# Performance work log

Measured on AMD Instinct MI355X. Metric: run time of the kernel, lower is better.

## Reference

```python
import jax, jax.numpy as jnp
import numpy as np

B, C, H, W = 64, 64, 64, 64
KD = 64  # kernel_dim == res == dim (required by the torch reshapes)


def _ln(t, g, b, eps=1e-5):
    mu = jnp.mean(t, axis=-1, keepdims=True)
    var = jnp.var(t, axis=-1, keepdims=True)
    return (t - mu) * jax.lax.rsqrt(var + eps) * g + b


def _cos_map(n, kd):
    i = jnp.arange(n, dtype=jnp.float32)[:, None]
    j = jnp.arange(kd, dtype=jnp.float32)[None, :]
    return jnp.cos(i * j * jnp.pi / n) / kd


def setup_inputs() -> dict:
    key = jax.random.key(0)
    ks = jax.random.split(key, 6)
    s = 0.02
    return {
        "x": jax.random.normal(ks[0], (B, C, H, W), jnp.float32),
        "freq_embed": jax.random.normal(ks[1], (H, W, C), jnp.float32),
        "g_k": jnp.ones((C,), jnp.float32), "b_k": jnp.zeros((C,), jnp.float32),
        "Wk": jax.random.normal(ks[2], (C, KD), jnp.float32) * s, "bk": jnp.zeros((KD,), jnp.float32),
        "g_z": jnp.ones((C,), jnp.float32), "b_z": jnp.zeros((C,), jnp.float32),
        "Wz": jax.random.normal(ks[3], (C, C), jnp.float32) * s, "bz": jnp.zeros((C,), jnp.float32),
        "g_o": jnp.ones((KD,), jnp.float32), "b_o": jnp.zeros((KD,), jnp.float32),
        "Wo": jax.random.normal(ks[4], (KD, C), jnp.float32) * s, "bo": jnp.zeros((C,), jnp.float32),
    }


def reference(x, freq_embed, g_k, b_k, Wk, bk, g_z, b_z, Wz, bz, g_o, b_o, Wo, bo):
    # x: (B,C,H,W) -> (B,H,W,C), matching the torch permute branch
    x = jnp.transpose(x, (0, 2, 3, 1))
    Bc, Hc, Wc, Cc = x.shape
    kd = Wk.shape[1]
    xin = x + freq_embed[None]                    # freq_embed broadcast over batch
    k = _ln(xin, g_k, b_k) @ Wk + bk              # (B,H,W,kd)
    z = _ln(freq_embed, g_z, b_z) @ Wz + bz       # to_k(freq_embed): (H,W,C)
    cosn = _cos_map(Hc, kd)                       # (H,kd)
    cosm = _cos_map(Wc, kd)                       # (W,kd)
    i = jnp.arange(Hc, dtype=jnp.float32)[:, None]
    j = jnp.arange(Wc, dtype=jnp.float32)[None, :]
    decay = (jnp.exp(-(i + j) / max(Hc, Wc)) / kd).astype(x.dtype)  # (H,W)
    wexp = decay[:, :, None] ** z                 # (H,W,C), decay > 0
    # separable forward DCT (two kernel-1 conv1d == two contractions)
    t = jnp.einsum('nh,bhwc->bnwc', cosn, k)
    t = jnp.einsum('mw,bnwc->bnmc', cosm, t)
    t = t * wexp[None]                            # exponential-decay spectral gate
    # separable inverse DCT
    t = jnp.einsum('nh,bnmc->bhmc', cosn, t)
    t = jnp.einsum('mw,bhmc->bhwc', cosm, t)
    out = _ln(t, g_o, b_o) * jax.nn.silu(z)[None]
    out = out @ Wo + bo
    return jnp.transpose(out, (0, 3, 1, 2))       # back to BCHW
```

## Files before the change

kernel.cpp:

```cpp
#include <hip/hip_runtime.h>


#define PL_ST 4160
#define TC_ST 4160

typedef __attribute__((ext_vector_type(8))) short short8;
typedef __attribute__((ext_vector_type(4))) float f32x4;
typedef __attribute__((ext_vector_type(4))) unsigned short us4;

__device__ __forceinline__ unsigned short bfrnd(float f) {
    unsigned int u = __builtin_bit_cast(unsigned int, f);
    u += 0x7FFFu + ((u >> 16) & 1u);
    return (unsigned short)(u >> 16);
}
__device__ __forceinline__ void bfsplit(float f, unsigned short& hi, unsigned short& lo) {
    unsigned short h = bfrnd(f);
    float fh = __builtin_bit_cast(float, (unsigned int)h << 16);
    hi = h;
    lo = bfrnd(f - fh);
}
__device__ __forceinline__ int swa(int row, int col) {
    return (row << 7) + (((col >> 3) ^ (row & 7)) << 4) + ((col & 7) << 1);
}
__device__ __forceinline__ short8 fragrd(const short* buf, int row, int kc) {
    int a = (row << 7) + ((kc ^ (row & 7)) << 4);
    return *(const short8*)((const char*)buf + a);
}
__device__ __forceinline__ f32x4 mm3(short8 ah, short8 al, short8 bh, short8 bl, f32x4 acc) {
    acc = __builtin_amdgcn_mfma_f32_16x16x32_bf16(ah, bh, acc, 0, 0, 0);
    acc = __builtin_amdgcn_mfma_f32_16x16x32_bf16(ah, bl, acc, 0, 0, 0);
    acc = __builtin_amdgcn_mfma_f32_16x16x32_bf16(al, bh, acc, 0, 0, 0);
    return acc;
}

__device__ __forceinline__ void mm_block(const short* Ah, const short* Al,
                                         const short* Bh, const short* Bl,
                                         int m0, int n0, int l15, int q,
                                         f32x4 (&acc)[2][2]) {
    const f32x4 zero = {0.f, 0.f, 0.f, 0.f};
    acc[0][0] = zero; acc[0][1] = zero; acc[1][0] = zero; acc[1][1] = zero;
    #pragma unroll
    for (int kb = 0; kb < 2; ++kb) {
        int kc = (kb << 2) + q;
        short8 a0h = fragrd(Ah, m0 + l15, kc);
        short8 a0l = fragrd(Al, m0 + l15, kc);
        short8 a1h = fragrd(Ah, m0 + 16 + l15, kc);
        short8 a1l = fragrd(Al, m0 + 16 + l15, kc);
        short8 b0h = fragrd(Bh, n0 + l15, kc);
        short8 b0l = fragrd(Bl, n0 + l15, kc);
        short8 b1h = fragrd(Bh, n0 + 16 + l15, kc);
        short8 b1l = fragrd(Bl, n0 + 16 + l15, kc);
        acc[0][0] = mm3(a0h, a0l, b0h, b0l, acc[0][0]);
        acc[0][1] = mm3(a0h, a0l, b1h, b1l, acc[0][1]);
        acc[1][0] = mm3(a1h, a1l, b0h, b0l, acc[1][0]);
        acc[1][1] = mm3(a1h, a1l, b1h, b1l, acc[1][1]);
    }
}

__device__ __forceinline__ void mm_block_regB(const short* Ah, const short* Al,
                                              const short8 (&bf)[2][2][2],
                                              int m0, int l15, int q,
                                              f32x4 (&acc)[2][2]) {
    const f32x4 zero = {0.f, 0.f, 0.f, 0.f};
    acc[0][0] = zero; acc[0][1] = zero; acc[1][0] = zero; acc[1][1] = zero;
    #pragma unroll
    for (int kb = 0; kb < 2; ++kb) {
        int kc = (kb << 2) + q;
        short8 a0h = fragrd(Ah, m0 + l15, kc);
        short8 a0l = fragrd(Al, m0 + l15, kc);
        short8 a1h = fragrd(Ah, m0 + 16 + l15, kc);
        short8 a1l = fragrd(Al, m0 + 16 + l15, kc);
        #pragma unroll
        for (int u = 0; u < 2; ++u) {
            acc[0][u] = mm3(a0h, a0l, bf[u][kb][0], bf[u][kb][1], acc[0][u]);
            acc[1][u] = mm3(a1h, a1l, bf[u][kb][0], bf[u][kb][1], acc[1][u]);
        }
    }
}

__global__ __launch_bounds__(256) void k_pre1(
    const float* __restrict__ g_k, const float* __restrict__ b_k,
    const float* __restrict__ Wk, const float* __restrict__ bk,
    const float* __restrict__ g_z, const float* __restrict__ b_z,
    const float* __restrict__ Wz, const float* __restrict__ bz,
    const float* __restrict__ Wo,
    unsigned short* __restrict__ WkTh, unsigned short* __restrict__ WkTl,
    float* __restrict__ su_k, float* __restrict__ v_k,
    unsigned short* __restrict__ WzTh, unsigned short* __restrict__ WzTl,
    float* __restrict__ su_z, float* __restrict__ v_z,
    unsigned short* __restrict__ WoTh, unsigned short* __restrict__ WoTl,
    unsigned short* __restrict__ cos_hi, unsigned short* __restrict__ cos_lo) {
    int t = threadIdx.x;
    if (blockIdx.x < 16) {
        int n = blockIdx.x * 4 + (t >> 6);
        int c = t & 63;
        unsigned short h_, l_;
        float wk = Wk[c * 64 + n];
        float a = g_k[c] * wk;
        bfsplit(a, h_, l_);
        WkTh[n * 64 + c] = h_;
        WkTl[n * 64 + c] = l_;
        float sa = a, sv = b_k[c] * wk;
        #pragma unroll
        for (int off = 32; off > 0; off >>= 1) {
            sa += __shfl_xor(sa, off, 64);
            sv += __shfl_xor(sv, off, 64);
        }
        if (c == 0) { su_k[n] = sa; v_k[n] = sv + bk[n]; }
        float wz = Wz[c * 64 + n];
        float az = g_z[c] * wz;
        bfsplit(az, h_, l_);
        WzTh[n * 64 + c] = h_;
        WzTl[n * 64 + c] = l_;
        float saz = az, svz = b_z[c] * wz;
        #pragma unroll
        for (int off = 32; off > 0; off >>= 1) {
            saz += __shfl_xor(saz, off, 64);
            svz += __shfl_xor(svz, off, 64);
        }
        if (c == 0) { su_z[n] = saz; v_z[n] = svz + bz[n]; }
        float wo = Wo[c * 64 + n];
        bfsplit(wo, h_, l_);
        WoTh[n * 64 + c] = h_;
        WoTl[n * 64 + c] = l_;
    } else {
        int idx = (blockIdx.x - 16) * 256 + t;
        int i = idx >> 6, j = idx & 63;
        float ang = (float)(i * j) * 3.14159265358979323846f * (1.0f / 64.0f);
        float v = cosf(ang) * (1.0f / 64.0f);
        unsigned short h_, l_;
        bfsplit(v, h_, l_);
        cos_hi[idx] = h_;
        cos_lo[idx] = l_;
    }
}

__global__ __launch_bounds__(256) void k_pre2(
    const float* __restrict__ freq,
    const unsigned short* __restrict__ WzTh_g, const unsigned short* __restrict__ WzTl_g,
    const float* __restrict__ su_z, const float* __restrict__ v_z,
    float* __restrict__ siluzT, float* __restrict__ wexpT,
    float* __restrict__ freqT) {
    __shared__ __align__(16) short Ah[4096], Al[4096], Bh[4096], Bl[4096];
    __shared__ float muS[64], rsS[64];
    __shared__ float tile[64][65];
    int t = threadIdx.x;
    if (blockIdx.x < 64) {
        int h = blockIdx.x;
        #pragma unroll
        for (int p = 0; p < 2; ++p) {
            int e = t + p * 256;
            int row = e >> 3, ch = e & 7;
            int a = (row << 7) + (((ch ^ (row & 7)) << 4));
            *(uint4*)((char*)Bh + a) = *(const uint4*)&WzTh_g[row * 64 + ch * 8];
            *(uint4*)((char*)Bl + a) = *(const uint4*)&WzTl_g[row * 64 + ch * 8];
        }
        int w = t >> 2, c0 = (t & 3) << 4;
        float4 fr[4];
        float s1 = 0.f, s2 = 0.f;
        #pragma unroll
        for (int i = 0; i < 4; ++i) {
            fr[i] = *(const float4*)&freq[(h * 64 + w) * 64 + c0 + 4 * i];
            s1 += fr[i].x + fr[i].y + fr[i].z + fr[i].w;
            s2 += fr[i].x * fr[i].x + fr[i].y * fr[i].y + fr[i].z * fr[i].z + fr[i].w * fr[i].w;
        }
        s1 += __shfl_xor(s1, 1, 64); s1 += __shfl_xor(s1, 2, 64);
        s2 += __shfl_xor(s2, 1, 64); s2 += __shfl_xor(s2, 2, 64);
        float mu = s1 * (1.0f / 64.0f);
        float var = s2 * (1.0f / 64.0f) - mu * mu;
        float rs = rsqrtf(var + 1e-5f);
        if ((t & 3) == 0) { muS[w] = mu; rsS[w] = rs; }
        const float* fp = (const float*)fr;
        #pragma unroll
        for (int i = 0; i < 4; ++i) {
            us4 hv, lv;
            #pragma unroll
            for (int r = 0; r < 4; ++r) {
                unsigned short h_, l_;
                bfsplit(fp[i * 4 + r], h_, l_);
                hv[r] = h_;
                lv[r] = l_;
            }
            int a = swa(w, c0 + 4 * i);
            *(us4*)((char*)Ah + a) = hv;
            *(us4*)((char*)Al + a) = lv;
        }
        __syncthreads();
        int lane = t & 63, wv = t >> 6;
        int q = lane >> 4, l15 = lane & 15;
        int m0 = (wv & 1) << 5, n0 = (wv >> 1) << 5;
        f32x4 acc[2][2];
        mm_block(Ah, Al, Bh, Bl, m0, n0, l15, q, acc);
        #pragma unroll
        for (int u = 0; u < 2; ++u) {
            int c = n0 + (u << 4) + l15;
            float suc = su_z[c], vc = v_z[c];
            #pragma unroll
            for (int ti = 0; ti < 2; ++ti) {
                int wb = m0 + (ti << 4) + (q << 2);
                float4 mu4 = *(const float4*)&muS[wb];
                float4 rs4 = *(const float4*)&rsS[wb];
                float4 sil, wx;
                #pragma unroll
                for (int r = 0; r < 4; ++r) {
                    float z = ((const float*)&rs4)[r] * (acc[ti][u][r] - ((const float*)&mu4)[r] * suc) + vc;
                    float lnd = -(float)(h + wb + r) * 0.015625f - 4.1588830833596718565f;
                    ((float*)&sil)[r] = z / (1.0f + expf(-z));
                    ((float*)&wx)[r] = expf(z * lnd);
                }
                size_t base = (size_t)c * TC_ST + h * 64 + wb;
                *(float4*)&siluzT[base] = sil;
                *(float4*)&wexpT[base] = wx;
            }
        }
    } else {
        int h = blockIdx.x - 64;
        int w = t >> 2, c0 = (t & 3) << 4;
        #pragma unroll
        for (int i = 0; i < 4; ++i)
            *(float4*)&tile[w][c0 + 4 * i] = *(const float4*)&freq[(h * 64 + w) * 64 + c0 + 4 * i];
        __syncthreads();
        int w0 = (t & 15) << 2;
        #pragma unroll
        for (int p = 0; p < 4; ++p) {
            int c = (t >> 4) + 16 * p;
            float4 fv = make_float4(tile[w0][c], tile[w0 + 1][c], tile[w0 + 2][c], tile[w0 + 3][c]);
            *(float4*)&freqT[(size_t)c * TC_ST + h * 64 + w0] = fv;
        }
    }
}

__global__ __launch_bounds__(256, 3) void k_k(
    const float* __restrict__ x, const float* __restrict__ freqT,
    const unsigned short* __restrict__ WkTh_g, const unsigned short* __restrict__ WkTl_g,
    const float* __restrict__ su_k, const float* __restrict__ v_k,
    float* __restrict__ planes) {
    __shared__ __align__(16) short Ah[2][4096], Al[2][4096];
    __shared__ __align__(16) float red1[4][64], red2[4][64];
    __shared__ float muS[64], rsS[64];
    int b = blockIdx.x >> 4, h0 = (blockIdx.x & 15) << 2;
    int t = threadIdx.x;
    int lane = t & 63, wv = t >> 6;
    int q = lane >> 4, l15 = lane & 15;
    int m0 = (wv & 1) << 5, n0 = (wv >> 1) << 5;
    short8 bf[2][2][2];
    #pragma unroll
    for (int u = 0; u < 2; ++u)
        #pragma unroll
        for (int kb = 0; kb < 2; ++kb) {
            int off = (n0 + (u << 4) + l15) * 64 + ((kb << 2) + q) * 8;
            bf[u][kb][0] = *(const short8*)&WkTh_g[off];
            bf[u][kb][1] = *(const short8*)&WkTl_g[off];
        }
    int g = t >> 4, w0 = (t & 15) << 2, c0 = g << 2;
    const float* xb = x + (size_t)b * 262144;
    float4 xr[2][4], fr[2][4];
    #pragma unroll
    for (int pi = 0; pi < 2; ++pi) {
        int h = h0 + pi;
        #pragma unroll
        for (int i = 0; i < 4; ++i) {
            xr[pi][i] = *(const float4*)&xb[(c0 + i) * 4096 + h * 64 + w0];
            fr[pi][i] = *(const float4*)&freqT[(size_t)(c0 + i) * TC_ST + h * 64 + w0];
        }
    }
    #pragma unroll
    for (int it = 0; it < 4; ++it) {
        int s = it & 1;
        int h = h0 + it;
        float4 vv[4];
        float4 s1 = {0, 0, 0, 0}, s2 = {0, 0, 0, 0};
        #pragma unroll
        for (int i = 0; i < 4; ++i) {
            float4 a = xr[s][i], f = fr[s][i];
            a.x += f.x; a.y += f.y; a.z += f.z; a.w += f.w;
            vv[i] = a;
            s1.x += a.x; s1.y += a.y; s1.z += a.z; s1.w += a.w;
            s2.x += a.x * a.x; s2.y += a.y * a.y; s2.z += a.z * a.z; s2.w += a.w * a.w;
        }
        const float* vp = (const float*)vv;
        #pragma unroll
        for (int j = 0; j < 4; ++j) {
            us4 hv, lv;
            #pragma unroll
            for (int r = 0; r < 4; ++r) {
                unsigned short h_, l_;
                bfsplit(vp[r * 4 + j], h_, l_);
                hv[r] = h_;
                lv[r] = l_;
            }
            int a = swa(w0 + j, c0);
            *(us4*)((char*)Ah[s] + a) = hv;
            *(us4*)((char*)Al[s] + a) = lv;
        }
        #pragma unroll
        for (int r = 0; r < 4; ++r) {
            float a1 = ((const float*)&s1)[r];
            float a2 = ((const float*)&s2)[r];
            a1 += __shfl_xor(a1, 16, 64); a1 += __shfl_xor(a1, 32, 64);
            a2 += __shfl_xor(a2, 16, 64); a2 += __shfl_xor(a2, 32, 64);
            ((float*)&s1)[r] = a1;
            ((float*)&s2)[r] = a2;
        }
        if (lane < 16) {
            *(float4*)&red1[wv][lane << 2] = s1;
            *(float4*)&red2[wv][lane << 2] = s2;
        }
        __syncthreads();
        if (t < 64) {
            float a1 = red1[0][t] + red1[1][t] + red1[2][t] + red1[3][t];
            float a2 = red2[0][t] + red2[1][t] + red2[2][t] + red2[3][t];
            float mu = a1 * (1.0f / 64.0f);
            float var = a2 * (1.0f / 64.0f) - mu * mu;
            muS[t] = mu; rsS[t] = rsqrtf(var + 1e-5f);
        }
        __syncthreads();
        if (it < 2) {
            int hn = h0 + it + 2;
            #pragma unroll
            for (int i = 0; i < 4; ++i) {
                xr[s][i] = *(const float4*)&xb[(c0 + i) * 4096 + hn * 64 + w0];
                fr[s][i] = *(const float4*)&freqT[(size_t)(c0 + i) * TC_ST + hn * 64 + w0];
            }
        }
        f32x4 acc[2][2];
        mm_block_regB(Ah[s], Al[s], bf, m0, l15, q, acc);
        float* slab = planes + (size_t)(b * 64 + h) * PL_ST;
        #pragma unroll
        for (int u = 0; u < 2; ++u) {
            int n = n0 + (u << 4) + l15;
            float sun = su_k[n], vn = v_k[n];
            #pragma unroll
            for (int ti = 0; ti < 2; ++ti) {
                int wb = m0 + (ti << 4) + (q << 2);
                float4 mu4 = *(const float4*)&muS[wb];
                float4 rs4 = *(const float4*)&rsS[wb];
                float4 o;
                o.x = rs4.x * (acc[ti][u][0] - mu4.x * sun) + vn;
                o.y = rs4.y * (acc[ti][u][1] - mu4.y * sun) + vn;
                o.z = rs4.z * (acc[ti][u][2] - mu4.z * sun) + vn;
                o.w = rs4.w * (acc[ti][u][3] - mu4.w * sun) + vn;
                *(float4*)&slab[n * 64 + wb] = o;
            }
        }
    }
}

__global__ __launch_bounds__(256, 4) void k_spec(
    float* __restrict__ planes,
    const unsigned short* __restrict__ cos_hi, const unsigned short* __restrict__ cos_lo,
    const float* __restrict__ wexpT) {
    __shared__ __align__(16) short Ch[4096], Cl[4096];
    __shared__ __align__(16) short Dmem[8192];
    short* Dh = Dmem;
    short* Dl = Dmem + 4096;
    int bid = blockIdx.x;
    int b = bid >> 6, c = bid & 63;
    float* pb = planes + (size_t)b * 64 * PL_ST + c * 64;
    const float* wx = wexpT + (size_t)c * TC_ST;
    int t = threadIdx.x;
    int lane = t & 63, wv = t >> 6;
    int q = lane >> 4, l15 = lane & 15;
    int m0 = (wv & 1) << 5, n0 = (wv >> 1) << 5;

    float wxr[2][2][4];
    #pragma unroll
    for (int ti = 0; ti < 2; ++ti)
        #pragma unroll
        for (int u = 0; u < 2; ++u)
            #pragma unroll
            for (int r = 0; r < 4; ++r)
                wxr[ti][u][r] = wx[(m0 + (ti << 4) + (q << 2) + r) * 64
                                   + n0 + (u << 4) + l15];

    {
        int r = t >> 2, cb = (t & 3) << 4;
        #pragma unroll
        for (int p = 0; p < 2; ++p) {
            int chunk = (cb >> 3) + p;
            int a = (r << 7) + (((chunk ^ (r & 7)) << 4));
            *(uint4*)((char*)Ch + a) = *(const uint4*)&cos_hi[r * 64 + cb + p * 8];
            *(uint4*)((char*)Cl + a) = *(const uint4*)&cos_lo[r * 64 + cb + p * 8];
        }
    }
    {
        int w = t & 63, h0 = (t >> 6) << 4;
        float v[16];
        #pragma unroll
        for (int j = 0; j < 16; ++j) v[j] = pb[(size_t)(h0 + j) * PL_ST + w];
        #pragma unroll
        for (int gg = 0; gg < 4; ++gg) {
            int col = h0 + (gg << 2);
            int a = swa(w, col);
            us4 hv, lv;
            #pragma unroll
            for (int r = 0; r < 4; ++r) {
                unsigned short h_, l_;
                bfsplit(v[(gg << 2) + r], h_, l_);
                hv[r] = h_;
                lv[r] = l_;
            }
            *(us4*)((char*)Dh + a) = hv;
            *(us4*)((char*)Dl + a) = lv;
        }
    }
    __syncthreads();

    short8 af[2][2][2];
    f32x4 acc[2][2];
    const f32x4 zacc = {0.f, 0.f, 0.f, 0.f};

#define LOAD_D(base)                                                          \
    _Pragma("unroll")                                                         \
    for (int tt = 0; tt < 2; ++tt)                                            \
        _Pragma("unroll")                                                     \
        for (int kb = 0; kb < 2; ++kb) {                                      \
            af[tt][kb][0] = fragrd(Dh, (base) + (tt << 4) + l15, (kb << 2) + q); \
            af[tt][kb][1] = fragrd(Dl, (base) + (tt << 4) + l15, (kb << 2) + q); \
        }

#define QMM_AC()                                                              \
    acc[0][0] = zacc; acc[0][1] = zacc; acc[1][0] = zacc; acc[1][1] = zacc;   \
    __builtin_amdgcn_s_setprio(1);                                            \
    _Pragma("unroll")                                                         \
    for (int kb = 0; kb < 2; ++kb) {                                          \
        int kc = (kb << 2) + q;                                               \
        short8 b0h = fragrd(Ch, n0 + l15, kc);                                \
        short8 b0l = fragrd(Cl, n0 + l15, kc);                                \
        short8 b1h = fragrd(Ch, n0 + 16 + l15, kc);                           \
        short8 b1l = fragrd(Cl, n0 + 16 + l15, kc);                           \
        acc[0][0] = mm3(af[0][kb][0], af[0][kb][1], b0h, b0l, acc[0][0]);     \
        acc[0][1] = mm3(af[0][kb][0], af[0][kb][1], b1h, b1l, acc[0][1]);     \
        acc[1][0] = mm3(af[1][kb][0], af[1][kb][1], b0h, b0l, acc[1][0]);     \
        acc[1][1] = mm3(af[1][kb][0], af[1][kb][1], b1h, b1l, acc[1][1]);     \
    }                                                                         \
    __builtin_amdgcn_s_setprio(0);

#define QMM_CA()                                                              \
    acc[0][0] = zacc; acc[0][1] = zacc; acc[1][0] = zacc; acc[1][1] = zacc;   \
    __builtin_amdgcn_s_setprio(1);                                            \
    _Pragma("unroll")                                                         \
    for (int kb = 0; kb < 2; ++kb) {                                          \
        int kc = (kb << 2) + q;                                               \
        short8 a0h = fragrd(Ch, m0 + l15, kc);                                \
        short8 a0l = fragrd(Cl, m0 + l15, kc);                                \
        short8 a1h = fragrd(Ch, m0 + 16 + l15, kc);                           \
        short8 a1l = fragrd(Cl, m0 + 16 + l15, kc);                           \
        acc[0][0] = mm3(a0h, a0l, af[0][kb][0], af[0][kb][1], acc[0][0]);     \
        acc[0][1] = mm3(a0h, a0l, af[1][kb][0], af[1][kb][1], acc[0][1]);     \
        acc[1][0] = mm3(a1h, a1l, af[0][kb][0], af[0][kb][1], acc[1][0]);     \
        acc[1][1] = mm3(a1h, a1l, af[1][kb][0], af[1][kb][1], acc[1][1]);     \
    }                                                                         \
    __builtin_amdgcn_s_setprio(0);

#define WB_T()                                                                \
    _Pragma("unroll")                                                         \
    for (int ti = 0; ti < 2; ++ti)                                            \
        _Pragma("unroll")                                                     \
        for (int u = 0; u < 2; ++u) {                                         \
            int row = n0 + (u << 4) + l15;                                    \
            int col = m0 + (ti << 4) + (q << 2);                              \
            int a = swa(row, col);                                            \
            us4 hv, lv;                                                       \
            _Pragma("unroll")                                                 \
            for (int r = 0; r < 4; ++r) {                                     \
                unsigned short h_, l_;                                        \
                bfsplit(acc[ti][u][r], h_, l_);                               \
                hv[r] = h_;                                                   \
                lv[r] = l_;                                                   \
            }                                                                 \
            *(us4*)((char*)Dh + a) = hv;                                      \
            *(us4*)((char*)Dl + a) = lv;                                      \
        }

    LOAD_D(m0)
    __syncthreads();
    QMM_AC()
    WB_T()
    __syncthreads();

    LOAD_D(m0)
    __syncthreads();
    QMM_AC()
    #pragma unroll
    for (int ti = 0; ti < 2; ++ti)
        #pragma unroll
        for (int u = 0; u < 2; ++u)
            #pragma unroll
            for (int r = 0; r < 4; ++r)
                acc[ti][u][r] *= wxr[ti][u][r];
    WB_T()
    __syncthreads();

    LOAD_D(n0)
    __syncthreads();
    QMM_CA()
    #pragma unroll
    for (int ti = 0; ti < 2; ++ti)
        #pragma unroll
        for (int u = 0; u < 2; ++u)
            #pragma unroll
            for (int r = 0; r < 4; ++r) {
                int row = m0 + (ti << 4) + (q << 2) + r;
                int col = n0 + (u << 4) + l15;
                int a = swa(row, col);
                unsigned short h_, l_;
                bfsplit(acc[ti][u][r], h_, l_);
                *(unsigned short*)((char*)Dh + a) = h_;
                *(unsigned short*)((char*)Dl + a) = l_;
            }
    __syncthreads();

    LOAD_D(m0)
    __syncthreads();
    QMM_AC()
    {
        float* Df = (float*)Dmem;
        #pragma unroll
        for (int ti = 0; ti < 2; ++ti)
            #pragma unroll
            for (int u = 0; u < 2; ++u)
                #pragma unroll
                for (int r = 0; r < 4; ++r) {
                    int h = m0 + (ti << 4) + (q << 2) + r;
                    int w = n0 + (u << 4) + l15;
                    Df[h * 64 + (w ^ (((h >> 2) & 3) << 4))] = acc[ti][u][r];
                }
    }
    __syncthreads();
    {
        const float* Df = (const float*)Dmem;
        int w = t & 63;
        #pragma unroll
        for (int j = 0; j < 16; ++j) {
            int row = j * 4 + wv;
            pb[(size_t)row * PL_ST + w] = Df[row * 64 + (w ^ (((row >> 2) & 3) << 4))];
        }
    }
#undef LOAD_D
#undef QMM_AC
#undef QMM_CA
#undef WB_T
}

__global__ __launch_bounds__(256, 3) void k_out(
    const float* __restrict__ planes, const float* __restrict__ siluzT,
    const float* __restrict__ g_o, const float* __restrict__ b_o,
    const unsigned short* __restrict__ WoTh_g, const unsigned short* __restrict__ WoTl_g,
    const float* __restrict__ bo, float* __restrict__ out) {
    __shared__ __align__(16) short Ah[2][4096], Al[2][4096];
    __shared__ __align__(16) float red1[4][64], red2[4][64];
    __shared__ float muS[64], rsS[64];
    int b = blockIdx.x >> 4, h0 = (blockIdx.x & 15) << 2;
    int t = threadIdx.x;
    int lane = t & 63, wv = t >> 6;
    int q = lane >> 4, l15 = lane & 15;
    int m0 = (wv & 1) << 5, n0 = (wv >> 1) << 5;
    short8 bf[2][2][2];
    #pragma unroll
    for (int u = 0; u < 2; ++u)
        #pragma unroll
        for (int kb = 0; kb < 2; ++kb) {
            int off = (n0 + (u << 4) + l15) * 64 + ((kb << 2) + q) * 8;
            bf[u][kb][0] = *(const short8*)&WoTh_g[off];
            bf[u][kb][1] = *(const short8*)&WoTl_g[off];
        }
    int g = t >> 4, w0 = (t & 15) << 2, c0 = g << 2;
    float4 pr[2][4], sz[2][4];
    #pragma unroll
    for (int pi = 0; pi < 2; ++pi) {
        int h = h0 + pi;
        const float* slab = planes + (size_t)(b * 64 + h) * PL_ST;
        #pragma unroll
        for (int i = 0; i < 4; ++i) {
            pr[pi][i] = *(const float4*)&slab[(c0 + i) * 64 + w0];
            sz[pi][i] = *(const float4*)&siluzT[(size_t)(c0 + i) * TC_ST + h * 64 + w0];
        }
    }
    #pragma unroll
    for (int it = 0; it < 4; ++it) {
        int s = it & 1;
        int h = h0 + it;
        float4 s1 = {0, 0, 0, 0}, s2 = {0, 0, 0, 0};
        #pragma unroll
        for (int i = 0; i < 4; ++i) {
            float4 tv = pr[s][i];
            s1.x += tv.x; s1.y += tv.y; s1.z += tv.z; s1.w += tv.w;
            s2.x += tv.x * tv.x; s2.y += tv.y * tv.y;
            s2.z += tv.z * tv.z; s2.w += tv.w * tv.w;
        }
        #pragma unroll
        for (int r = 0; r < 4; ++r) {
            float a1 = ((const float*)&s1)[r];
            float a2 = ((const float*)&s2)[r];
            a1 += __shfl_xor(a1, 16, 64); a1 += __shfl_xor(a1, 32, 64);
            a2 += __shfl_xor(a2, 16, 64); a2 += __shfl_xor(a2, 32, 64);
            ((float*)&s1)[r] = a1;
            ((float*)&s2)[r] = a2;
        }
        if (lane < 16) {
            *(float4*)&red1[wv][lane << 2] = s1;
            *(float4*)&red2[wv][lane << 2] = s2;
        }
        __syncthreads();
        if (t < 64) {
            float a1 = red1[0][t] + red1[1][t] + red1[2][t] + red1[3][t];
            float a2 = red2[0][t] + red2[1][t] + red2[2][t] + red2[3][t];
            float mu = a1 * (1.0f / 64.0f);
            float var = a2 * (1.0f / 64.0f) - mu * mu;
            muS[t] = mu; rsS[t] = rsqrtf(var + 1e-5f);
        }
        __syncthreads();
        {
            float4 mu4 = *(const float4*)&muS[w0];
            float4 rs4 = *(const float4*)&rsS[w0];
            float4 vr[4];
            #pragma unroll
            for (int i = 0; i < 4; ++i) {
                int cc = c0 + i;
                float go = g_o[cc], boc = b_o[cc];
                float4 tv = pr[s][i], sv = sz[s][i];
                vr[i].x = ((tv.x - mu4.x) * rs4.x * go + boc) * sv.x;
                vr[i].y = ((tv.y - mu4.y) * rs4.y * go + boc) * sv.y;
                vr[i].z = ((tv.z - mu4.z) * rs4.z * go + boc) * sv.z;
                vr[i].w = ((tv.w - mu4.w) * rs4.w * go + boc) * sv.w;
            }
            const float* vp = (const float*)vr;
            #pragma unroll
            for (int j = 0; j < 4; ++j) {
                us4 hv, lv;
                #pragma unroll
                for (int r = 0; r < 4; ++r) {
                    unsigned short h_, l_;
                    bfsplit(vp[r * 4 + j], h_, l_);
                    hv[r] = h_;
                    lv[r] = l_;
                }
                int a = swa(w0 + j, c0);
                *(us4*)((char*)Ah[s] + a) = hv;
                *(us4*)((char*)Al[s] + a) = lv;
            }
        }
        if (it < 2) {
            int hn = h0 + it + 2;
            const float* slab = planes + (size_t)(b * 64 + hn) * PL_ST;
            #pragma unroll
            for (int i = 0; i < 4; ++i) {
                pr[s][i] = *(const float4*)&slab[(c0 + i) * 64 + w0];
                sz[s][i] = *(const float4*)&siluzT[(size_t)(c0 + i) * TC_ST + hn * 64 + w0];
            }
        }
        __syncthreads();
        f32x4 acc[2][2];
        mm_block_regB(Ah[s], Al[s], bf, m0, l15, q, acc);
        #pragma unroll
        for (int u = 0; u < 2; ++u) {
            int o_ = n0 + (u << 4) + l15;
            float bov = bo[o_];
            #pragma unroll
            for (int ti = 0; ti < 2; ++ti) {
                int wb = m0 + (ti << 4) + (q << 2);
                float4 o;
                o.x = acc[ti][u][0] + bov;
                o.y = acc[ti][u][1] + bov;
                o.z = acc[ti][u][2] + bov;
                o.w = acc[ti][u][3] + bov;
                *(float4*)&out[((size_t)(b * 64 + o_) * 64 + h) * 64 + wb] = o;
            }
        }
    }
}

extern "C" void kernel_launch(void* const* d_in, const int* in_sizes, int n_in,
                              void* d_out, int out_size, void* d_ws, size_t ws_size,
                              hipStream_t stream) {
    const float* x    = (const float*)d_in[0];
    const float* freq = (const float*)d_in[1];
    const float* g_k  = (const float*)d_in[2];
    const float* b_k  = (const float*)d_in[3];
    const float* Wk   = (const float*)d_in[4];
    const float* bk   = (const float*)d_in[5];
    const float* g_z  = (const float*)d_in[6];
    const float* b_z  = (const float*)d_in[7];
    const float* Wz   = (const float*)d_in[8];
    const float* bz   = (const float*)d_in[9];
    const float* g_o  = (const float*)d_in[10];
    const float* b_o  = (const float*)d_in[11];
    const float* Wo   = (const float*)d_in[12];
    const float* bo   = (const float*)d_in[13];
    float* out = (float*)d_out;

    float* ws = (float*)d_ws;
    float* planes = ws;
    float* siluzT = planes + (size_t)4096 * PL_ST;
    float* wexpT  = siluzT + (size_t)64 * TC_ST;
    float* freqT  = wexpT + (size_t)64 * TC_ST;
    float* su_k   = freqT + (size_t)64 * TC_ST;
    float* v_k    = su_k + 64;
    float* su_z   = v_k + 64;
    float* v_z    = su_z + 64;
    unsigned short* cos_hi = (unsigned short*)(v_z + 64);
    unsigned short* cos_lo = cos_hi + 4096;
    unsigned short* WkTh = cos_lo + 4096;
    unsigned short* WkTl = WkTh + 4096;
    unsigned short* WzTh = WkTl + 4096;
    unsigned short* WzTl = WzTh + 4096;
    unsigned short* WoTh = WzTl + 4096;
    unsigned short* WoTl = WoTh + 4096;

    k_pre1<<<32, 256, 0, stream>>>(g_k, b_k, Wk, bk, g_z, b_z, Wz, bz, Wo,
                                   WkTh, WkTl, su_k, v_k, WzTh, WzTl, su_z, v_z,
                                   WoTh, WoTl, cos_hi, cos_lo);
    k_pre2<<<128, 256, 0, stream>>>(freq, WzTh, WzTl, su_z, v_z, siluzT, wexpT, freqT);
    k_k<<<1024, 256, 0, stream>>>(x, freqT, WkTh, WkTl, su_k, v_k, planes);
    k_spec<<<4096, 256, 0, stream>>>(planes, cos_hi, cos_lo, wexpT);
    k_out<<<1024, 256, 0, stream>>>(planes, siluzT, g_o, b_o, WoTh, WoTl, bo, out);
}
```

Baseline: 223.1 us.

## Add lo*lo MFMA term and simplify k_k to one row per block

Every split-bf16 matmul helper now issues a fourth MFMA for the low*low product, so the emulated fp32 products are more exact. Each MFMA sequence costs a third more instructions. Separately, k_k drops its 4-row, double-buffered, prefetching loop. It now processes a single h row per block across 4096 blocks, which gives more parallelism and less LDS per block but removes load/compute overlap inside a block.

```diff
diff --git a/kernel.cpp b/kernel.cpp
--- a/kernel.cpp
+++ b/kernel.cpp
@@ -26,10 +26,11 @@
     int a = (row << 7) + ((kc ^ (row & 7)) << 4);
     return *(const short8*)((const char*)buf + a);
 }
-__device__ __forceinline__ f32x4 mm3(short8 ah, short8 al, short8 bh, short8 bl, f32x4 acc) {
+__device__ __forceinline__ f32x4 mm4(short8 ah, short8 al, short8 bh, short8 bl, f32x4 acc) {
     acc = __builtin_amdgcn_mfma_f32_16x16x32_bf16(ah, bh, acc, 0, 0, 0);
     acc = __builtin_amdgcn_mfma_f32_16x16x32_bf16(ah, bl, acc, 0, 0, 0);
     acc = __builtin_amdgcn_mfma_f32_16x16x32_bf16(al, bh, acc, 0, 0, 0);
+    acc = __builtin_amdgcn_mfma_f32_16x16x32_bf16(al, bl, acc, 0, 0, 0);
     return acc;
 }
 
@@ -50,10 +51,10 @@
         short8 b0l = fragrd(Bl, n0 + l15, kc);
         short8 b1h = fragrd(Bh, n0 + 16 + l15, kc);
         short8 b1l = fragrd(Bl, n0 + 16 + l15, kc);
-        acc[0][0] = mm3(a0h, a0l, b0h, b0l, acc[0][0]);
-        acc[0][1] = mm3(a0h, a0l, b1h, b1l, acc[0][1]);
-        acc[1][0] = mm3(a1h, a1l, b0h, b0l, acc[1][0]);
-        acc[1][1] = mm3(a1h, a1l, b1h, b1l, acc[1][1]);
+        acc[0][0] = mm4(a0h, a0l, b0h, b0l, acc[0][0]);
+        acc[0][1] = mm4(a0h, a0l, b1h, b1l, acc[0][1]);
+        acc[1][0] = mm4(a1h, a1l, b0h, b0l, acc[1][0]);
+        acc[1][1] = mm4(a1h, a1l, b1h, b1l, acc[1][1]);
     }
 }
 
@@ -72,8 +73,8 @@
         short8 a1l = fragrd(Al, m0 + 16 + l15, kc);
         #pragma unroll
         for (int u = 0; u < 2; ++u) {
-            acc[0][u] = mm3(a0h, a0l, bf[u][kb][0], bf[u][kb][1], acc[0][u]);
-            acc[1][u] = mm3(a1h, a1l, bf[u][kb][0], bf[u][kb][1], acc[1][u]);
+            acc[0][u] = mm4(a0h, a0l, bf[u][kb][0], bf[u][kb][1], acc[0][u]);
+            acc[1][u] = mm4(a1h, a1l, bf[u][kb][0], bf[u][kb][1], acc[1][u]);
         }
     }
 }
@@ -235,10 +236,10 @@
     const unsigned short* __restrict__ WkTh_g, const unsigned short* __restrict__ WkTl_g,
     const float* __restrict__ su_k, const float* __restrict__ v_k,
     float* __restrict__ planes) {
-    __shared__ __align__(16) short Ah[2][4096], Al[2][4096];
+    __shared__ __align__(16) short Ah[4096], Al[4096];
     __shared__ __align__(16) float red1[4][64], red2[4][64];
     __shared__ float muS[64], rsS[64];
-    int b = blockIdx.x >> 4, h0 = (blockIdx.x & 15) << 2;
+    int b = blockIdx.x >> 6, h = blockIdx.x & 63;
     int t = threadIdx.x;
     int lane = t & 63, wv = t >> 6;
     int q = lane >> 4, l15 = lane & 15;
@@ -253,95 +254,73 @@
             bf[u][kb][1] = *(const short8*)&WkTl_g[off];
         }
     int g = t >> 4, w0 = (t & 15) << 2, c0 = g << 2;
-    const float* xb = x + (size_t)b * 262144;
-    float4 xr[2][4], fr[2][4];
-    #pragma unroll
-    for (int pi = 0; pi < 2; ++pi) {
-        int h = h0 + pi;
-        #pragma unroll
-        for (int i = 0; i < 4; ++i) {
-            xr[pi][i] = *(const float4*)&xb[(c0 + i) * 4096 + h * 64 + w0];
-            fr[pi][i] = *(const float4*)&freqT[(size_t)(c0 + i) * TC_ST + h * 64 + w0];
-        }
-    }
-    #pragma unroll
-    for (int it = 0; it < 4; ++it) {
-        int s = it & 1;
-        int h = h0 + it;
-        float4 vv[4];
-        float4 s1 = {0, 0, 0, 0}, s2 = {0, 0, 0, 0};
-        #pragma unroll
-        for (int i = 0; i < 4; ++i) {
-            float4 a = xr[s][i], f = fr[s][i];
-            a.x += f.x; a.y += f.y; a.z += f.z; a.w += f.w;
-            vv[i] = a;
-            s1.x += a.x; s1.y += a.y; s1.z += a.z; s1.w += a.w;
-            s2.x += a.x * a.x; s2.y += a.y * a.y; s2.z += a.z * a.z; s2.w += a.w * a.w;
-        }
-        const float* vp = (const float*)vv;
-        #pragma unroll
-        for (int j = 0; j < 4; ++j) {
-            us4 hv, lv;
-            #pragma unroll
-            for (int r = 0; r < 4; ++r) {
-                unsigned short h_, l_;
-                bfsplit(vp[r * 4 + j], h_, l_);
-                hv[r] = h_;
-                lv[r] = l_;
-            }
-            int a = swa(w0 + j, c0);
-            *(us4*)((char*)Ah[s] + a) = hv;
-            *(us4*)((char*)Al[s] + a) = lv;
-        }
+    const float* xb = x + (size_t)b * 262144 + h * 64;
+    float4 vv[4];
+    float4 s1 = {0, 0, 0, 0}, s2 = {0, 0, 0, 0};
+    #pragma unroll
+    for (int i = 0; i < 4; ++i) {
+        float4 a = *(const float4*)&xb[(c0 + i) * 4096 + w0];
+        float4 f = *(const float4*)&freqT[(size_t)(c0 + i) * TC_ST + h * 64 + w0];
+        a.x += f.x; a.y += f.y; a.z += f.z; a.w += f.w;
+        vv[i] = a;
+        s1.x += a.x; s1.y += a.y; s1.z += a.z; s1.w += a.w;
+        s2.x += a.x * a.x; s2.y += a.y * a.y; s2.z += a.z * a.z; s2.w += a.w * a.w;
+    }
+    const float* vp = (const float*)vv;
+    #pragma unroll
+    for (int j = 0; j < 4; ++j) {
+        us4 hv, lv;
         #pragma unroll
         for (int r = 0; r < 4; ++r) {
-            float a1 = ((const float*)&s1)[r];
-            float a2 = ((const float*)&s2)[r];
-            a1 += __shfl_xor(a1, 16, 64); a1 += __shfl_xor(a1, 32, 64);
-            a2 += __shfl_xor(a2, 16, 64); a2 += __shfl_xor(a2, 32, 64);
-            ((float*)&s1)[r] = a1;
-            ((float*)&s2)[r] = a2;
-        }
-        if (lane < 16) {
-            *(float4*)&red1[wv][lane << 2] = s1;
-            *(float4*)&red2[wv][lane << 2] = s2;
-        }
-        __syncthreads();
-        if (t < 64) {
-            float a1 = red1[0][t] + red1[1][t] + red1[2][t] + red1[3][t];
-            float a2 = red2[0][t] + red2[1][t] + red2[2][t] + red2[3][t];
-            float mu = a1 * (1.0f / 64.0f);
-            float var = a2 * (1.0f / 64.0f) - mu * mu;
-            muS[t] = mu; rsS[t] = rsqrtf(var + 1e-5f);
-        }
-        __syncthreads();
-        if (it < 2) {
-            int hn = h0 + it + 2;
-            #pragma unroll
-            for (int i = 0; i < 4; ++i) {
-                xr[s][i] = *(const float4*)&xb[(c0 + i) * 4096 + hn * 64 + w0];
-                fr[s][i] = *(const float4*)&freqT[(size_t)(c0 + i) * TC_ST + hn * 64 + w0];
-            }
-        }
-        f32x4 acc[2][2];
-        mm_block_regB(Ah[s], Al[s], bf, m0, l15, q, acc);
-        float* slab = planes + (size_t)(b * 64 + h) * PL_ST;
-        #pragma unroll
-        for (int u = 0; u < 2; ++u) {
-            int n = n0 + (u << 4) + l15;
-            float sun = su_k[n], vn = v_k[n];
-            #pragma unroll
-            for (int ti = 0; ti < 2; ++ti) {
-                int wb = m0 + (ti << 4) + (q << 2);
-                float4 mu4 = *(const float4*)&muS[wb];
-                float4 rs4 = *(const float4*)&rsS[wb];
-                float4 o;
-                o.x = rs4.x * (acc[ti][u][0] - mu4.x * sun) + vn;
-                o.y = rs4.y * (acc[ti][u][1] - mu4.y * sun) + vn;
-                o.z = rs4.z * (acc[ti][u][2] - mu4.z * sun) + vn;
-                o.w = rs4.w * (acc[ti][u][3] - mu4.w * sun) + vn;
-                *(float4*)&slab[n * 64 + wb] = o;
-            }
+            unsigned short h_, l_;
+            bfsplit(vp[r * 4 + j], h_, l_);
+            hv[r] = h_;
+            lv[r] = l_;
+        }
+        int a = swa(w0 + j, c0);
+        *(us4*)((char*)Ah + a) = hv;
+        *(us4*)((char*)Al + a) = lv;
+    }
+    #pragma unroll
+    for (int r = 0; r < 4; ++r) {
+        float a1 = ((const float*)&s1)[r];
+        float a2 = ((const float*)&s2)[r];
+        a1 += __shfl_xor(a1, 16, 64); a1 += __shfl_xor(a1, 32, 64);
+        a2 += __shfl_xor(a2, 16, 64); a2 += __shfl_xor(a2, 32, 64);
+        ((float*)&s1)[r] = a1;
+        ((float*)&s2)[r] = a2;
+    }
+    if (lane < 16) {
+        *(float4*)&red1[wv][lane << 2] = s1;
+        *(float4*)&red2[wv][lane << 2] = s2;
+    }
+    __syncthreads();
+    if (t < 64) {
+        float a1 = red1[0][t] + red1[1][t] + red1[2][t] + red1[3][t];
+        float a2 = red2[0][t] + red2[1][t] + red2[2][t] + red2[3][t];
+        float mu = a1 * (1.0f / 64.0f);
+        float var = a2 * (1.0f / 64.0f) - mu * mu;
+        muS[t] = mu; rsS[t] = rsqrtf(var + 1e-5f);
+    }
+    __syncthreads();
+    f32x4 acc[2][2];
+    mm_block_regB(Ah, Al, bf, m0, l15, q, acc);
+    float* slab = planes + (size_t)(b * 64 + h) * PL_ST;
+    #pragma unroll
+    for (int u = 0; u < 2; ++u) {
+        int n = n0 + (u << 4) + l15;
+        float sun = su_k[n], vn = v_k[n];
+        #pragma unroll
+        for (int ti = 0; ti < 2; ++ti) {
+            int wb = m0 + (ti << 4) + (q << 2);
+            float4 mu4 = *(const float4*)&muS[wb];
+            float4 rs4 = *(const float4*)&rsS[wb];
+            float4 o;
+            o.x = rs4.x * (acc[ti][u][0] - mu4.x * sun) + vn;
+            o.y = rs4.y * (acc[ti][u][1] - mu4.y * sun) + vn;
+            o.z = rs4.z * (acc[ti][u][2] - mu4.z * sun) + vn;
+            o.w = rs4.w * (acc[ti][u][3] - mu4.w * sun) + vn;
+            *(float4*)&slab[n * 64 + wb] = o;
         }
     }
 }
@@ -429,10 +408,10 @@
         short8 b0l = fragrd(Cl, n0 + l15, kc);                                \
         short8 b1h = fragrd(Ch, n0 + 16 + l15, kc);                           \
         short8 b1l = fragrd(Cl, n0 + 16 + l15, kc);                           \
-        acc[0][0] = mm3(af[0][kb][0], af[0][kb][1], b0h, b0l, acc[0][0]);     \
-        acc[0][1] = mm3(af[0][kb][0], af[0][kb][1], b1h, b1l, acc[0][1]);     \
-        acc[1][0] = mm3(af[1][kb][0], af[1][kb][1], b0h, b0l, acc[1][0]);     \
-        acc[1][1] = mm3(af[1][kb][0], af[1][kb][1], b1h, b1l, acc[1][1]);     \
+        acc[0][0] = mm4(af[0][kb][0], af[0][kb][1], b0h, b0l, acc[0][0]);     \
+        acc[0][1] = mm4(af[0][kb][0], af[0][kb][1], b1h, b1l, acc[0][1]);     \
+        acc[1][0] = mm4(af[1][kb][0], af[1][kb][1], b0h, b0l, acc[1][0]);     \
+        acc[1][1] = mm4(af[1][kb][0], af[1][kb][1], b1h, b1l, acc[1][1]);     \
     }                                                                         \
     __builtin_amdgcn_s_setprio(0);
 
@@ -446,10 +425,10 @@
         short8 a0l = fragrd(Cl, m0 + l15, kc);                                \
         short8 a1h = fragrd(Ch, m0 + 16 + l15, kc);                           \
         short8 a1l = fragrd(Cl, m0 + 16 + l15, kc);                           \
-        acc[0][0] = mm3(a0h, a0l, af[0][kb][0], af[0][kb][1], acc[0][0]);     \
-        acc[0][1] = mm3(a0h, a0l, af[1][kb][0], af[1][kb][1], acc[0][1]);     \
-        acc[1][0] = mm3(a1h, a1l, af[0][kb][0], af[0][kb][1], acc[1][0]);     \
-        acc[1][1] = mm3(a1h, a1l, af[1][kb][0], af[1][kb][1], acc[1][1]);     \
+        acc[0][0] = mm4(a0h, a0l, af[0][kb][0], af[0][kb][1], acc[0][0]);     \
+        acc[0][1] = mm4(a0h, a0l, af[1][kb][0], af[1][kb][1], acc[0][1]);     \
+        acc[1][0] = mm4(a1h, a1l, af[0][kb][0], af[0][kb][1], acc[1][0]);     \
+        acc[1][1] = mm4(a1h, a1l, af[1][kb][0], af[1][kb][1], acc[1][1]);     \
     }                                                                         \
     __builtin_amdgcn_s_setprio(0);
 
@@ -712,7 +691,7 @@
                                    WkTh, WkTl, su_k, v_k, WzTh, WzTl, su_z, v_z,
                                    WoTh, WoTl, cos_hi, cos_lo);
     k_pre2<<<128, 256, 0, stream>>>(freq, WzTh, WzTl, su_z, v_z, siluzT, wexpT, freqT);
-    k_k<<<1024, 256, 0, stream>>>(x, freqT, WkTh, WkTl, su_k, v_k, planes);
+    k_k<<<4096, 256, 0, stream>>>(x, freqT, WkTh, WkTl, su_k, v_k, planes);
     k_spec<<<4096, 256, 0, stream>>>(planes, cos_hi, cos_lo, wexpT);
     k_out<<<1024, 256, 0, stream>>>(planes, siluzT, g_o, b_o, WoTh, WoTl, bo, out);
 }
```

After: 230.0 us. 1.03x slower.
